# Optimization experiments

Measured on AMD Instinct MI355X. Metric: run time of the kernel, lower is better.

The kernel has to match this reference:

```python
import jax, jax.numpy as jnp
import numpy as np

NBATCH, NUP, NDOWN, NMO, NCONF = 8192, 8, 8, 32, 64


def setup_inputs() -> dict:
    key = jax.random.key(0)
    k1, k2, k3, k4 = jax.random.split(key, 4)
    MO = jax.random.normal(k1, (NBATCH, NUP + NDOWN, NMO), dtype=jnp.float32)
    d2MO = jax.random.normal(k2, (NBATCH, NUP + NDOWN, NMO), dtype=jnp.float32)
    # each config = 8 distinct MO column indices per spin (distinct -> invertible A)
    configs_up = jnp.argsort(jax.random.uniform(k3, (NCONF, NMO)), axis=1)[:, :NUP].astype(jnp.int32)
    configs_down = jnp.argsort(jax.random.uniform(k4, (NCONF, NMO)), axis=1)[:, :NDOWN].astype(jnp.int32)
    return {"MO": MO, "d2MO": d2MO, "configs_up": configs_up, "configs_down": configs_down}


def _gather(M, elec_idx, cols):
    # M: (B, nelec, nmo) -> select electron rows then per-config MO columns
    Ms = M[:, elec_idx, :]                  # (B, n, nmo)
    A = jnp.take(Ms, cols, axis=2)          # (B, n, C, n)
    return jnp.transpose(A, (0, 2, 1, 3))   # (B, C, n, n)


def reference(MO, d2MO, configs_up, configs_down):
    nup = configs_up.shape[1]
    ndown = configs_down.shape[1]
    iup = jnp.arange(nup)
    idown = jnp.arange(nup, nup + ndown)

    Aup = _gather(MO, iup, configs_up)       # (B, C, nup, nup)
    Adn = _gather(MO, idown, configs_down)   # (B, C, ndown, ndown)
    d2up = _gather(d2MO, iup, configs_up)
    d2dn = _gather(d2MO, idown, configs_down)

    iAup = jnp.linalg.inv(Aup)
    iAdn = jnp.linalg.inv(Adn)

    # btrace(iA @ d2A) = sum_ij iA[i,j] * d2A[j,i]
    tr = lambda X, Y: jnp.einsum('bcij,bcji->bc', X, Y)
    out = tr(iAup, d2up) + tr(iAdn, d2dn)    # (B, C)

    # return_local_energy=False branch: multiply by product of determinants
    pd = jnp.linalg.det(Aup) * jnp.linalg.det(Adn)
    return -0.5 * out * pd
```

## Files before the change

### kernel.cpp

```cpp
#include <hip/hip_runtime.h>

#define NBATCH 8192
#define NELEC  16
#define NMO    32
#define NCONF  64
#define NS     8
#define TSTR   20
#define TSZ    (NMO * TSTR)
#define TSTRH  24
#define TSZH   (NMO * TSTRH)

typedef float    v2f   __attribute__((ext_vector_type(2)));
typedef _Float16 half8 __attribute__((ext_vector_type(8)));
typedef _Float16 half4 __attribute__((ext_vector_type(4)));

__device__ __forceinline__ v2f pkfma(v2f a, v2f b, v2f c) {
#if __has_builtin(__builtin_elementwise_fma)
    return __builtin_elementwise_fma(a, b, c);
#else
    return a * b + c;
#endif
}
__device__ __forceinline__ v2f bc2(float s) { return (v2f){s, s}; }
__device__ __forceinline__ float getel2(const v2f (&R)[4], int j) {
    return (j & 1) ? R[j >> 1].y : R[j >> 1].x;
}
__device__ __forceinline__ void setel2(v2f (&R)[4], int j, float v) {
    if (j & 1) R[j >> 1].y = v; else R[j >> 1].x = v;
}

__device__ __forceinline__ void solve8T(const float* __restrict__ MOT,
                                        const _Float16* __restrict__ D2T,
                                        const int (&cols)[NS], int eoff,
                                        float& det_out, float& tr_out)
{
    v2f A2[NS][4];
    #pragma unroll
    for (int j = 0; j < NS; ++j) {
        const float4* pa = (const float4*)(MOT + cols[j] * TSTR + eoff);
        float4 a0 = pa[0], a1 = pa[1];
        A2[j][0] = (v2f){a0.x, a0.y};
        A2[j][1] = (v2f){a0.z, a0.w};
        A2[j][2] = (v2f){a1.x, a1.y};
        A2[j][3] = (v2f){a1.z, a1.w};
    }

    float det = 1.0f;
    #pragma unroll
    for (int k = 0; k < NS; ++k) {
        float ukk = getel2(A2[k], k);
        det *= ukk;
        float pinv = __builtin_amdgcn_rcpf(ukk);
        #pragma unroll
        for (int r = k + 1; r < NS; ++r) {
            float m = getel2(A2[r], k) * pinv;
            v2f m2 = bc2(m);
            #pragma unroll
            for (int p = (k + 1) >> 1; p < 4; ++p)
                A2[r][p] = pkfma(-m2, A2[k][p], A2[r][p]);
            setel2(A2[r], k, m);
        }
        setel2(A2[k], k, pinv);
    }

    float tr0 = 0.0f, tr1 = 0.0f;
    #pragma unroll
    for (int t = 0; t < 4; ++t) {
        const int k0 = 2 * t, k1 = 2 * t + 1;

        half8 hd0 = *(const half8*)(D2T + cols[k0] * TSTRH + eoff);
        half8 hd1 = *(const half8*)(D2T + cols[k1] * TSTRH + eoff);

        v2f z[NS];
        z[k0] = (v2f){1.0f, 0.0f};
        z[k1] = (v2f){-getel2(A2[k1], k0), 1.0f};
        #pragma unroll
        for (int i = k1 + 1; i < NS; ++i) {
            v2f a = (v2f){0.0f, 0.0f};
            #pragma unroll
            for (int j = k0; j < i; ++j)
                a = pkfma(bc2(getel2(A2[i], j)), z[j], a);
            z[i] = -a;
        }

        #pragma unroll
        for (int i = NS - 1; i >= 0; --i) {
            v2f a = (i >= k0) ? z[i] : (v2f){0.0f, 0.0f};
            #pragma unroll
            for (int c2 = i + 1; c2 < NS; ++c2)
                a = pkfma(-bc2(getel2(A2[i], c2)), z[c2], a);
            z[i] = a * bc2(getel2(A2[i], i));
        }

        #pragma unroll
        for (int i = 0; i < NS; ++i) {
            tr0 = fmaf(z[i].x, (float)hd0[i], tr0);
            tr1 = fmaf(z[i].y, (float)hd1[i], tr1);
        }
    }

    det_out = det;
    tr_out  = tr0 + tr1;
}

__global__ __launch_bounds__(256, 3)
void kp_dh_kernel(const float* __restrict__ MO,
                  const float* __restrict__ d2MO,
                  const int*   __restrict__ cfg_up,
                  const int*   __restrict__ cfg_dn,
                  float*       __restrict__ out)
{
    __shared__ float    smemA[2][TSZ];
    __shared__ _Float16 smemD[2][TSZH];
    __shared__ float    xtr [2][NCONF];
    __shared__ float    xdet[2][NCONF];

    const int tid  = threadIdx.x;
    const int half = tid >> 7;
    const int u    = tid & 127;
    const int b    = blockIdx.x * 2 + half;

    float*    MOT = smemA[half];
    _Float16* D2T = smemD[half];

    const float* MOb = MO   + (size_t)b * NELEC * NMO;
    const float* d2b = d2MO + (size_t)b * NELEC * NMO;

    {
        const int c  = u & 31;
        const int r0 = (u >> 5) << 2;
        const float* pa = MOb + r0 * NMO + c;
        const float* pd = d2b + r0 * NMO + c;
        float a0 = pa[0 * NMO], a1 = pa[1 * NMO], a2 = pa[2 * NMO], a3 = pa[3 * NMO];
        float d0 = pd[0 * NMO], d1 = pd[1 * NMO], d2 = pd[2 * NMO], d3 = pd[3 * NMO];
        *(float4*)(MOT + c * TSTR + r0) = make_float4(a0, a1, a2, a3);
        *(half4*)(D2T + c * TSTRH + r0) =
            (half4){(_Float16)d0, (_Float16)d1, (_Float16)d2, (_Float16)d3};
    }

    const int s    = (tid >> 6) & 1;
    const int cidx = tid & 63;
    const int* cfg = s ? cfg_dn : cfg_up;
    int4 q0 = ((const int4*)cfg)[cidx * 2 + 0];
    int4 q1 = ((const int4*)cfg)[cidx * 2 + 1];
    const int cols[NS] = {q0.x, q0.y, q0.z, q0.w, q1.x, q1.y, q1.z, q1.w};

    __syncthreads();

    float det, tr;
    solve8T(MOT, D2T, cols, s * NS, det, tr);

    if (s) { xtr[half][cidx] = tr; xdet[half][cidx] = det; }
    __syncthreads();
    if (!s)
        out[(size_t)b * NCONF + cidx] =
            -0.5f * (tr + xtr[half][cidx]) * det * xdet[half][cidx];
}

extern "C" void kernel_launch(void* const* d_in, const int* in_sizes, int n_in,
                              void* d_out, int out_size, void* d_ws, size_t ws_size,
                              hipStream_t stream)
{
    const float* MO     = (const float*)d_in[0];
    const float* d2MO   = (const float*)d_in[1];
    const int*   cfg_up = (const int*)d_in[2];
    const int*   cfg_dn = (const int*)d_in[3];
    float* out = (float*)d_out;

    dim3 grid(NBATCH / 2);
    dim3 block(256);
    kp_dh_kernel<<<grid, block, 0, stream>>>(MO, d2MO, cfg_up, cfg_dn, out);
}
```

Measured before the change: 88.64 us.

## Process 8 batches per block with double-buffered LDS prefetch of next pair

Each block now loops over four pairs of batch elements instead of handling one pair. While the current pair is solved, the next pair's MO and d2MO tiles are loaded from global memory into registers and then written into a second LDS buffer, which hides load latency behind compute. The config indices are loaded once per block, and there are fewer blocks. In exchange the grid shrinks to 1024 blocks, which lowers parallelism on a large GPU, and register and LDS pressure per thread goes up.

Result: no change. 90.27 us (+1.8%).

```diff
diff --git a/kernel.cpp b/kernel.cpp
--- a/kernel.cpp
+++ b/kernel.cpp
@@ -9,6 +9,8 @@
 #define TSZ    (NMO * TSTR)
 #define TSTRH  24
 #define TSZH   (NMO * TSTRH)
+#define BPB    8
+#define NR     (BPB / 2)
 
 typedef float    v2f   __attribute__((ext_vector_type(2)));
 typedef _Float16 half8 __attribute__((ext_vector_type(8)));
@@ -110,33 +112,21 @@
                   const int*   __restrict__ cfg_dn,
                   float*       __restrict__ out)
 {
-    __shared__ float    smemA[2][TSZ];
-    __shared__ _Float16 smemD[2][TSZH];
-    __shared__ float    xtr [2][NCONF];
-    __shared__ float    xdet[2][NCONF];
+    __shared__ float    smemA[2][2][TSZ];
+    __shared__ _Float16 smemD[2][2][TSZH];
+    __shared__ float    xtr [2][2][NCONF];
+    __shared__ float    xdet[2][2][NCONF];
 
     const int tid  = threadIdx.x;
     const int half = tid >> 7;
     const int u    = tid & 127;
-    const int b    = blockIdx.x * 2 + half;
+    const int b0   = blockIdx.x * BPB;
 
-    float*    MOT = smemA[half];
-    _Float16* D2T = smemD[half];
-
-    const float* MOb = MO   + (size_t)b * NELEC * NMO;
-    const float* d2b = d2MO + (size_t)b * NELEC * NMO;
-
-    {
-        const int c  = u & 31;
-        const int r0 = (u >> 5) << 2;
-        const float* pa = MOb + r0 * NMO + c;
-        const float* pd = d2b + r0 * NMO + c;
-        float a0 = pa[0 * NMO], a1 = pa[1 * NMO], a2 = pa[2 * NMO], a3 = pa[3 * NMO];
-        float d0 = pd[0 * NMO], d1 = pd[1 * NMO], d2 = pd[2 * NMO], d3 = pd[3 * NMO];
-        *(float4*)(MOT + c * TSTR + r0) = make_float4(a0, a1, a2, a3);
-        *(half4*)(D2T + c * TSTRH + r0) =
-            (half4){(_Float16)d0, (_Float16)d1, (_Float16)d2, (_Float16)d3};
-    }
+    const int c  = u & 31;
+    const int r0 = (u >> 5) << 2;
+    const size_t goff = (size_t)(b0 + half) * NELEC * NMO + r0 * NMO + c;
+    const float* pa = MO   + goff;
+    const float* pd = d2MO + goff;
 
     const int s    = (tid >> 6) & 1;
     const int cidx = tid & 63;
@@ -145,16 +135,46 @@
     int4 q1 = ((const int4*)cfg)[cidx * 2 + 1];
     const int cols[NS] = {q0.x, q0.y, q0.z, q0.w, q1.x, q1.y, q1.z, q1.w};
 
+    {
+        float a0 = pa[0 * NMO], a1 = pa[1 * NMO], a2 = pa[2 * NMO], a3 = pa[3 * NMO];
+        float d0 = pd[0 * NMO], d1 = pd[1 * NMO], d2 = pd[2 * NMO], d3 = pd[3 * NMO];
+        *(float4*)(smemA[0][half] + c * TSTR + r0) = make_float4(a0, a1, a2, a3);
+        *(half4*)(smemD[0][half] + c * TSTRH + r0) =
+            (half4){(_Float16)d0, (_Float16)d1, (_Float16)d2, (_Float16)d3};
+    }
     __syncthreads();
 
-    float det, tr;
-    solve8T(MOT, D2T, cols, s * NS, det, tr);
+    #pragma unroll
+    for (int r = 0; r < NR; ++r) {
+        const int cur = r & 1;
 
-    if (s) { xtr[half][cidx] = tr; xdet[half][cidx] = det; }
-    __syncthreads();
-    if (!s)
-        out[(size_t)b * NCONF + cidx] =
-            -0.5f * (tr + xtr[half][cidx]) * det * xdet[half][cidx];
+        float a0, a1, a2, a3, d0, d1, d2, d3;
+        if (r + 1 < NR) {
+            const size_t st = (size_t)2 * NELEC * NMO * (r + 1);
+            a0 = pa[st + 0 * NMO]; a1 = pa[st + 1 * NMO];
+            a2 = pa[st + 2 * NMO]; a3 = pa[st + 3 * NMO];
+            d0 = pd[st + 0 * NMO]; d1 = pd[st + 1 * NMO];
+            d2 = pd[st + 2 * NMO]; d3 = pd[st + 3 * NMO];
+        }
+
+        float det, tr;
+        solve8T(smemA[cur][half], smemD[cur][half], cols, s * NS, det, tr);
+
+        if (r + 1 < NR) {
+            *(float4*)(smemA[cur ^ 1][half] + c * TSTR + r0) =
+                make_float4(a0, a1, a2, a3);
+            *(half4*)(smemD[cur ^ 1][half] + c * TSTRH + r0) =
+                (half4){(_Float16)d0, (_Float16)d1, (_Float16)d2, (_Float16)d3};
+        }
+
+        if (s) { xtr[cur][half][cidx] = tr; xdet[cur][half][cidx] = det; }
+        __syncthreads();
+        if (!s) {
+            const int b = b0 + 2 * r + half;
+            out[(size_t)b * NCONF + cidx] =
+                -0.5f * (tr + xtr[cur][half][cidx]) * det * xdet[cur][half][cidx];
+        }
+    }
 }
 
 extern "C" void kernel_launch(void* const* d_in, const int* in_sizes, int n_in,
@@ -167,7 +187,7 @@
     const int*   cfg_dn = (const int*)d_in[3];
     float* out = (float*)d_out;
 
-    dim3 grid(NBATCH / 2);
+    dim3 grid(NBATCH / BPB);
     dim3 block(256);
     kp_dh_kernel<<<grid, block, 0, stream>>>(MO, d2MO, cfg_up, cfg_dn, out);
 }
```
